# Kernel optimization log

Hardware: AMD Instinct MI355X
Metric: run time of the kernel (lower is better)

## Reference

```python
import jax, jax.numpy as jnp
import numpy as np

DT = 0.1
B, L, IN_SZ, MEM = 64, 2048, 128, 256


def setup_inputs() -> dict:
    key = jax.random.key(0)
    ks = jax.random.split(key, 13)
    u = jax.random.normal(ks[0], (B, L, IN_SZ), dtype=jnp.float32)
    s_in = 1.0 / np.sqrt(IN_SZ)
    s_h = 1.0 / np.sqrt(MEM)
    def w_in(k):
        return jax.random.normal(k, (MEM, IN_SZ), dtype=jnp.float32) * s_in
    def w_h(k):
        return jax.random.normal(k, (MEM, MEM), dtype=jnp.float32) * s_h
    return {
        "u": u,
        "Wia": w_in(ks[1]), "Wha": w_h(ks[2]),
        "Wib": w_in(ks[3]), "Whb": w_h(ks[4]),
        "Wic": w_in(ks[5]), "Whc": w_h(ks[6]),
        "Wid": w_in(ks[7]), "Whd": w_h(ks[8]),
        "Wie": w_in(ks[9]), "Whe": w_h(ks[10]),
        "Wio": w_in(ks[11]),
    }


def _run(u, Wia, Wha, Wib, Whb, Wic, Whc, Wid, Whd, Wie, Whe, Wio):
    # Precompute all 6 input projections once: [L, B, MEM] each (time-major for scan)
    Win = jnp.stack([Wia, Wib, Wic, Wid, Wie, Wio], axis=0)  # [6, MEM, IN]
    xproj = jnp.einsum("blk,gmk->lgbm", u, Win)  # [L, 6, B, MEM]

    hf0 = jnp.zeros((u.shape[0], Wha.shape[0]), dtype=u.dtype)
    hs0 = jnp.zeros_like(hf0)

    def step(carry, xs):
        hf, hs = carry
        xa, xb, xc, xd, xe, xo = xs[0], xs[1], xs[2], xs[3], xs[4], xs[5]
        a = 1.0 + jnp.tanh(xa + hf @ Wha.T)
        b = 1.5 * (1.0 + jnp.tanh(xb + hf @ Whb.T))
        c = 3.0 * DT + (1.0 - 3.0 * DT) * jax.nn.sigmoid(xc + hf @ Whc.T)
        d = 0.3 * DT * jax.nn.sigmoid(xd + hf @ Whd.T)
        e = 1.0 + jax.nn.sigmoid(xe + hf @ Whe.T)
        hfn = (1.0 - c) * hf + c * jnp.tanh(xo + (a + b * hf * hf - hs) * hf)
        hsn = hs * (1.0 - d) + d * (e * hf) ** 4
        return (hfn, hsn), hfn

    _, hseq = jax.lax.scan(step, (hf0, hs0), xproj)  # [L, B, MEM]
    hseq = jnp.transpose(hseq, (1, 0, 2))  # [B, L, MEM]
    return hseq


def reference(u, Wia, Wha, Wib, Whb, Wic, Whc, Wid, Whd, Wie, Whe, Wio):
    hseq = _run(u, Wia, Wha, Wib, Whb, Wic, Whc, Wid, Whd, Wie, Whe, Wio)
    return hseq, hseq[:, -1:, :]
```

## Files before the change

kernel.cpp:

```cpp
#include <hip/hip_runtime.h>
#include <hip/hip_fp16.h>

#define L_SEQ 2048
#define N_B   64
#define IN_K  128
#define MEM_N 256

typedef float    f32x4 __attribute__((ext_vector_type(4)));
typedef _Float16 f16x8 __attribute__((ext_vector_type(8)));
typedef unsigned u32x4 __attribute__((ext_vector_type(4)));

__device__ __forceinline__ float rcp_f(float x) { return __builtin_amdgcn_rcpf(x); }
__device__ __forceinline__ float tanh_f(float x) {
    return 1.0f - 2.0f * rcp_f(__expf(2.0f * x) + 1.0f);
}
__device__ __forceinline__ float sig_f(float x) {
    return rcp_f(1.0f + __expf(-x));
}

__device__ __forceinline__ void split8(const float* v, f16x8& hi, f16x8& lo) {
#pragma unroll
    for (int i = 0; i < 8; ++i) {
        _Float16 h = (_Float16)v[i];
        hi[i] = h;
        lo[i] = (_Float16)(v[i] - (float)h);
    }
}

__global__ void __launch_bounds__(256, 1)
befrc_scan(const float* __restrict__ u,
           const float* __restrict__ Wia, const float* __restrict__ Wha,
           const float* __restrict__ Wib, const float* __restrict__ Whb,
           const float* __restrict__ Wic, const float* __restrict__ Whc,
           const float* __restrict__ Wid, const float* __restrict__ Whd,
           const float* __restrict__ Wie, const float* __restrict__ Whe,
           const float* __restrict__ Wio,
           float* __restrict__ out,
           unsigned long long* __restrict__ pubq)
{
    const int wg  = blockIdx.x;
    const int g   = wg & 3;
    const int s   = wg >> 2;
    const int tid = threadIdx.x;
    const int w   = tid >> 6;
    const int l   = tid & 63;
    const int lq  = l >> 4;
    const int lr  = l & 15;

    __shared__ __align__(16) float red[2][6][4][16][20];

    const float* Wi[6] = {Wia, Wib, Wic, Wid, Wie, Wio};
    const float* Wh[5] = {Wha, Whb, Whc, Whd, Whe};

    const int mrow = s * 16 + lr;
    f16x8 whf_hi[5][2], whf_lo[5][2];
#pragma unroll
    for (int gg = 0; gg < 5; ++gg) {
#pragma unroll
        for (int cc = 0; cc < 2; ++cc) {
            const int k0 = (2 * w + cc) * 32 + lq * 4;
            const float* p = Wh[gg] + mrow * MEM_N + k0;
            float4 f0 = *(const float4*)p;
            float4 f1 = *(const float4*)(p + 16);
            float v[8] = {f0.x, f0.y, f0.z, f0.w, f1.x, f1.y, f1.z, f1.w};
            split8(v, whf_hi[gg][cc], whf_lo[gg][cc]);
        }
    }
    f16x8 wif_hi[6], wif_lo[6];
#pragma unroll
    for (int gg = 0; gg < 6; ++gg) {
        const int k0 = w * 32 + lq * 4;
        const float* p = Wi[gg] + mrow * IN_K + k0;
        float4 f0 = *(const float4*)p;
        float4 f1 = *(const float4*)(p + 16);
        float v[8] = {f0.x, f0.y, f0.z, f0.w, f1.x, f1.y, f1.z, f1.w};
        split8(v, wif_hi[gg], wif_lo[gg]);
    }

    const int eb    = tid >> 4;
    const int em    = tid & 15;
    const int bglob = g * 16 + eb;
    const int mglob = s * 16 + em;
    float hf_loc = 0.0f, hs_loc = 0.0f;

    const int  bfrag  = g * 16 + lr;
    const long u_base = (long)bfrag * L_SEQ * IN_K + w * 32 + lq * 4;
    const int  k0a    = (2 * w + 0) * 32 + lq * 4;
    const int  k0b    = (2 * w + 1) * 32 + lq * 4;

    u32x4 ua, ub2;
    {
        const float* up = u + u_base;
        asm volatile(
            "global_load_dwordx4 %0, %2, off\n\t"
            "global_load_dwordx4 %1, %3, off"
            : "=v"(ua), "=v"(ub2)
            : "v"(up), "v"(up + 16)
            : "memory");
    }

    float* const out_row = out + (long)bglob * L_SEQ * MEM_N + mglob;

#pragma clang loop unroll(disable)
    for (int t = 0; t < L_SEQ; ++t) {
        u32x4 r0, r1, r2, r3, r4, r5, r6, r7;
        {
            const unsigned tgt = (unsigned)t;
            const unsigned long long* pb =
                pubq + (size_t)(t & 1) * N_B * MEM_N + (size_t)bfrag * MEM_N;
            const unsigned long long* p0 = pb + k0a;
            const unsigned long long* p1 = pb + k0a + 16;
            const unsigned long long* p2 = pb + k0b;
            const unsigned long long* p3 = pb + k0b + 16;
            int spins = 0;
            for (;;) {
                asm volatile(
                    "global_load_dwordx4 %0, %8, off sc0 sc1\n\t"
                    "global_load_dwordx4 %1, %8, off offset:16 sc0 sc1\n\t"
                    "global_load_dwordx4 %2, %9, off sc0 sc1\n\t"
                    "global_load_dwordx4 %3, %9, off offset:16 sc0 sc1\n\t"
                    "global_load_dwordx4 %4, %10, off sc0 sc1\n\t"
                    "global_load_dwordx4 %5, %10, off offset:16 sc0 sc1\n\t"
                    "global_load_dwordx4 %6, %11, off sc0 sc1\n\t"
                    "global_load_dwordx4 %7, %11, off offset:16 sc0 sc1\n\t"
                    "s_waitcnt vmcnt(0)"
                    : "=v"(r0), "=v"(r1), "=v"(r2), "=v"(r3),
                      "=v"(r4), "=v"(r5), "=v"(r6), "=v"(r7)
                    : "v"(p0), "v"(p1), "v"(p2), "v"(p3)
                    : "memory");
                int ok = (r0[1] == tgt) & (r0[3] == tgt) & (r1[1] == tgt) & (r1[3] == tgt)
                       & (r2[1] == tgt) & (r2[3] == tgt) & (r3[1] == tgt) & (r3[3] == tgt)
                       & (r4[1] == tgt) & (r4[3] == tgt) & (r5[1] == tgt) & (r5[3] == tgt)
                       & (r6[1] == tgt) & (r6[3] == tgt) & (r7[1] == tgt) & (r7[3] == tgt);
                if (__all(ok) || ++spins > (1 << 17)) break;
            }
        }
        __builtin_amdgcn_sched_barrier(0);

        f32x4 acc[6];
#pragma unroll
        for (int gg = 0; gg < 6; ++gg) acc[gg] = (f32x4){0.f, 0.f, 0.f, 0.f};
        {
            float4 f0 = __builtin_bit_cast(float4, ua);
            float4 f1 = __builtin_bit_cast(float4, ub2);
            float v[8] = {f0.x, f0.y, f0.z, f0.w, f1.x, f1.y, f1.z, f1.w};
            f16x8 uh, ul;
            split8(v, uh, ul);
#pragma unroll
            for (int gg = 0; gg < 6; ++gg) {
                acc[gg] = __builtin_amdgcn_mfma_f32_16x16x32_f16(wif_hi[gg], uh, acc[gg], 0, 0, 0);
                acc[gg] = __builtin_amdgcn_mfma_f32_16x16x32_f16(wif_hi[gg], ul, acc[gg], 0, 0, 0);
                acc[gg] = __builtin_amdgcn_mfma_f32_16x16x32_f16(wif_lo[gg], uh, acc[gg], 0, 0, 0);
            }
        }

        {
            const float* up = u + u_base + (long)((t + 1 < L_SEQ) ? t + 1 : t) * IN_K;
            asm volatile(
                "global_load_dwordx4 %0, %2, off\n\t"
                "global_load_dwordx4 %1, %3, off"
                : "=v"(ua), "=v"(ub2)
                : "v"(up), "v"(up + 16)
                : "memory");
        }

        unsigned pay[16] = {r0[0], r0[2], r1[0], r1[2], r2[0], r2[2], r3[0], r3[2],
                            r4[0], r4[2], r5[0], r5[2], r6[0], r6[2], r7[0], r7[2]};
#pragma unroll
        for (int cc = 0; cc < 2; ++cc) {
            f16x8 hb_hi, hb_lo;
#pragma unroll
            for (int j = 0; j < 8; ++j) {
                const unsigned p = pay[cc * 8 + j];
                hb_hi[j] = __builtin_bit_cast(_Float16, (unsigned short)(p & 0xffff));
                hb_lo[j] = __builtin_bit_cast(_Float16, (unsigned short)(p >> 16));
            }
#pragma unroll
            for (int gg = 0; gg < 5; ++gg) {
                acc[gg] = __builtin_amdgcn_mfma_f32_16x16x32_f16(whf_hi[gg][cc], hb_hi, acc[gg], 0, 0, 0);
                acc[gg] = __builtin_amdgcn_mfma_f32_16x16x32_f16(whf_hi[gg][cc], hb_lo, acc[gg], 0, 0, 0);
                acc[gg] = __builtin_amdgcn_mfma_f32_16x16x32_f16(whf_lo[gg][cc], hb_hi, acc[gg], 0, 0, 0);
            }
        }

        const int pb2 = t & 1;
#pragma unroll
        for (int gg = 0; gg < 6; ++gg)
            *(f32x4*)&red[pb2][gg][w][lr][lq * 4] = acc[gg];
        asm volatile("s_waitcnt lgkmcnt(0)\n\ts_barrier" ::: "memory");
        __builtin_amdgcn_sched_barrier(0);

        float pre0, pre1, pre2, pre5;
        pre0 = red[pb2][0][0][eb][em] + red[pb2][0][1][eb][em]
             + red[pb2][0][2][eb][em] + red[pb2][0][3][eb][em];
        pre1 = red[pb2][1][0][eb][em] + red[pb2][1][1][eb][em]
             + red[pb2][1][2][eb][em] + red[pb2][1][3][eb][em];
        pre2 = red[pb2][2][0][eb][em] + red[pb2][2][1][eb][em]
             + red[pb2][2][2][eb][em] + red[pb2][2][3][eb][em];
        pre5 = red[pb2][5][0][eb][em] + red[pb2][5][1][eb][em]
             + red[pb2][5][2][eb][em] + red[pb2][5][3][eb][em];

        const float hf_old = hf_loc, hs_old = hs_loc;
        {
            const float av  = 1.0f + tanh_f(pre0);
            const float bv  = 1.5f * (1.0f + tanh_f(pre1));
            const float cv  = 0.3f  + 0.7f * sig_f(pre2);
            const float arg = pre5 + (av + bv * hf_old * hf_old - hs_old) * hf_old;
            hf_loc = (1.0f - cv) * hf_old + cv * tanh_f(arg);
        }
        {
            const _Float16 ph = (_Float16)hf_loc;
            const _Float16 pl = (_Float16)(hf_loc - (float)ph);
            const unsigned paw = (unsigned)__builtin_bit_cast(unsigned short, ph)
                               | ((unsigned)__builtin_bit_cast(unsigned short, pl) << 16);
            const unsigned long long val = ((unsigned long long)(unsigned)(t + 1) << 32) | paw;
            const size_t po = (size_t)((t + 1) & 1) * N_B * MEM_N
                            + (size_t)bglob * MEM_N + mglob;
            __hip_atomic_store(pubq + po, val, __ATOMIC_RELAXED, __HIP_MEMORY_SCOPE_AGENT);
        }

        {
            const float pre3 = red[pb2][3][0][eb][em] + red[pb2][3][1][eb][em]
                             + red[pb2][3][2][eb][em] + red[pb2][3][3][eb][em];
            const float pre4 = red[pb2][4][0][eb][em] + red[pb2][4][1][eb][em]
                             + red[pb2][4][2][eb][em] + red[pb2][4][3][eb][em];
            const float dv  = 0.03f * sig_f(pre3);
            const float ev  = 1.0f + sig_f(pre4);
            const float eh  = ev * hf_old;
            const float eh2 = eh * eh;
            hs_loc = hs_old * (1.0f - dv) + dv * (eh2 * eh2);
        }
        out_row[(long)t * MEM_N] = hf_loc;
    }

    out[(long)N_B * L_SEQ * MEM_N + (long)bglob * MEM_N + mglob] = hf_loc;
}

extern "C" void kernel_launch(void* const* d_in, const int* in_sizes, int n_in,
                              void* d_out, int out_size, void* d_ws, size_t ws_size,
                              hipStream_t stream) {
    (void)in_sizes; (void)n_in; (void)out_size; (void)ws_size;
    const float* u   = (const float*)d_in[0];
    const float* Wia = (const float*)d_in[1];
    const float* Wha = (const float*)d_in[2];
    const float* Wib = (const float*)d_in[3];
    const float* Whb = (const float*)d_in[4];
    const float* Wic = (const float*)d_in[5];
    const float* Whc = (const float*)d_in[6];
    const float* Wid = (const float*)d_in[7];
    const float* Whd = (const float*)d_in[8];
    const float* Wie = (const float*)d_in[9];
    const float* Whe = (const float*)d_in[10];
    const float* Wio = (const float*)d_in[11];

    float* out = (float*)d_out;
    unsigned long long* pubq = (unsigned long long*)d_ws;

    hipMemsetAsync(d_ws, 0, (size_t)2 * N_B * MEM_N * sizeof(unsigned long long), stream);

    befrc_scan<<<dim3(64), dim3(256), 0, stream>>>(
        u, Wia, Wha, Wib, Whb, Wic, Whc, Wid, Whd, Wie, Whe, Wio,
        out, pubq);
}
```

Measured before the change: 5.616 ms.

## Place workgroups on one XCC and use L2-coherent polling when co-located

The kernel now launches 512 workgroups and keeps only every eighth one, which tends to place the working groups on the same XCC. At startup the groups run a probe handshake that reads the XCC id and checks cross-group store visibility. If all peers in a batch group share one XCC, the per-step exchange switches from system-coherent (sc0 sc1) loads and atomic stores to sc0-only loads and plain stores, which avoids the slower cross-die coherence path. The output store of each step is also deferred into the next iteration so it sits off the critical path. The risks are the fragile placement assumption and the extra startup handshake; the kernel falls back to the old path if the check fails.

```diff
diff --git a/kernel.cpp b/kernel.cpp
--- a/kernel.cpp
+++ b/kernel.cpp
@@ -27,7 +27,7 @@
     }
 }
 
-__global__ void __launch_bounds__(256, 1)
+__global__ void __launch_bounds__(256, 2)
 befrc_scan(const float* __restrict__ u,
            const float* __restrict__ Wia, const float* __restrict__ Wha,
            const float* __restrict__ Wib, const float* __restrict__ Whb,
@@ -36,11 +36,14 @@
            const float* __restrict__ Wie, const float* __restrict__ Whe,
            const float* __restrict__ Wio,
            float* __restrict__ out,
-           unsigned long long* __restrict__ pubq)
+           unsigned long long* __restrict__ pubq,
+           unsigned* __restrict__ ctrl,
+           unsigned* __restrict__ probe)
 {
-    const int wg  = blockIdx.x;
-    const int g   = wg & 3;
-    const int s   = wg >> 2;
+    if (blockIdx.x & 7) return;
+    const int rwg = blockIdx.x >> 3;
+    const int g   = rwg & 3;
+    const int s   = rwg >> 2;
     const int tid = threadIdx.x;
     const int w   = tid >> 6;
     const int l   = tid & 63;
@@ -48,6 +51,49 @@
     const int lr  = l & 15;
 
     __shared__ __align__(16) float red[2][6][4][16][20];
+    __shared__ int s_fast;
+
+    unsigned xcc;
+    asm volatile("s_getreg_b32 %0, hwreg(HW_REG_XCC_ID)" : "=s"(xcc));
+    int ok = 1;
+    {
+        unsigned* myslot = probe + (unsigned)rwg * 16;
+        const unsigned* peer = probe + (unsigned)(g + 4 * (l & 15)) * 16;
+        for (int r = 1; r <= 4; ++r) {
+            if (tid == 0)
+                asm volatile("global_store_dword %0, %1, off"
+                             :: "v"(myslot), "v"(r) : "memory");
+            if (w == 0) {
+                int good = 0;
+                for (int it = 0; it < 2048; ++it) {
+                    unsigned v;
+                    asm volatile("global_load_dword %0, %1, off sc0\n\t"
+                                 "s_waitcnt vmcnt(0)"
+                                 : "=v"(v) : "v"(peer) : "memory");
+                    if (__all((int)(l >= 16 || v >= (unsigned)r))) { good = 1; break; }
+                }
+                ok &= good;
+            }
+        }
+    }
+    if (tid == 0)
+        __hip_atomic_store(&ctrl[rwg],
+                           0x10000u | ((unsigned)(ok & 1) << 8) | (xcc & 0xffu),
+                           __ATOMIC_RELEASE, __HIP_MEMORY_SCOPE_AGENT);
+    if (w == 0) {
+        unsigned v;
+        for (;;) {
+            v = __hip_atomic_load(&ctrl[g + 4 * (l & 15)],
+                                  __ATOMIC_ACQUIRE, __HIP_MEMORY_SCOPE_AGENT);
+            if (__all((int)((v & 0x10000u) != 0))) break;
+            __builtin_amdgcn_s_sleep(2);
+        }
+        const unsigned ref = __builtin_amdgcn_readfirstlane(v);
+        const int f = (__all((int)(v == ref)) && ((ref >> 8) & 1)) ? 1 : 0;
+        if (tid == 0) s_fast = f;
+    }
+    __syncthreads();
+    const bool fast = (s_fast != 0);
 
     const float* Wi[6] = {Wia, Wib, Wic, Wid, Wie, Wio};
     const float* Wh[5] = {Wha, Whb, Whc, Whd, Whe};
@@ -81,7 +127,7 @@
     const int em    = tid & 15;
     const int bglob = g * 16 + eb;
     const int mglob = s * 16 + em;
-    float hf_loc = 0.0f, hs_loc = 0.0f;
+    float hf_loc = 0.0f, hs_loc = 0.0f, h_prev = 0.0f;
 
     const int  bfrag  = g * 16 + lr;
     const long u_base = (long)bfrag * L_SEQ * IN_K + w * 32 + lq * 4;
@@ -113,29 +159,55 @@
             const unsigned long long* p2 = pb + k0b;
             const unsigned long long* p3 = pb + k0b + 16;
             int spins = 0;
-            for (;;) {
-                asm volatile(
-                    "global_load_dwordx4 %0, %8, off sc0 sc1\n\t"
-                    "global_load_dwordx4 %1, %8, off offset:16 sc0 sc1\n\t"
-                    "global_load_dwordx4 %2, %9, off sc0 sc1\n\t"
-                    "global_load_dwordx4 %3, %9, off offset:16 sc0 sc1\n\t"
-                    "global_load_dwordx4 %4, %10, off sc0 sc1\n\t"
-                    "global_load_dwordx4 %5, %10, off offset:16 sc0 sc1\n\t"
-                    "global_load_dwordx4 %6, %11, off sc0 sc1\n\t"
-                    "global_load_dwordx4 %7, %11, off offset:16 sc0 sc1\n\t"
-                    "s_waitcnt vmcnt(0)"
-                    : "=v"(r0), "=v"(r1), "=v"(r2), "=v"(r3),
-                      "=v"(r4), "=v"(r5), "=v"(r6), "=v"(r7)
-                    : "v"(p0), "v"(p1), "v"(p2), "v"(p3)
-                    : "memory");
-                int ok = (r0[1] == tgt) & (r0[3] == tgt) & (r1[1] == tgt) & (r1[3] == tgt)
-                       & (r2[1] == tgt) & (r2[3] == tgt) & (r3[1] == tgt) & (r3[3] == tgt)
-                       & (r4[1] == tgt) & (r4[3] == tgt) & (r5[1] == tgt) & (r5[3] == tgt)
-                       & (r6[1] == tgt) & (r6[3] == tgt) & (r7[1] == tgt) & (r7[3] == tgt);
-                if (__all(ok) || ++spins > (1 << 17)) break;
+            if (fast) {
+                for (;;) {
+                    asm volatile(
+                        "global_load_dwordx4 %0, %8, off sc0\n\t"
+                        "global_load_dwordx4 %1, %8, off offset:16 sc0\n\t"
+                        "global_load_dwordx4 %2, %9, off sc0\n\t"
+                        "global_load_dwordx4 %3, %9, off offset:16 sc0\n\t"
+                        "global_load_dwordx4 %4, %10, off sc0\n\t"
+                        "global_load_dwordx4 %5, %10, off offset:16 sc0\n\t"
+                        "global_load_dwordx4 %6, %11, off sc0\n\t"
+                        "global_load_dwordx4 %7, %11, off offset:16 sc0\n\t"
+                        "s_waitcnt vmcnt(0)"
+                        : "=v"(r0), "=v"(r1), "=v"(r2), "=v"(r3),
+                          "=v"(r4), "=v"(r5), "=v"(r6), "=v"(r7)
+                        : "v"(p0), "v"(p1), "v"(p2), "v"(p3)
+                        : "memory");
+                    int ok2 = (r0[1] == tgt) & (r0[3] == tgt) & (r1[1] == tgt) & (r1[3] == tgt)
+                            & (r2[1] == tgt) & (r2[3] == tgt) & (r3[1] == tgt) & (r3[3] == tgt)
+                            & (r4[1] == tgt) & (r4[3] == tgt) & (r5[1] == tgt) & (r5[3] == tgt)
+                            & (r6[1] == tgt) & (r6[3] == tgt) & (r7[1] == tgt) & (r7[3] == tgt);
+                    if (__all(ok2) || ++spins > (1 << 20)) break;
+                }
+            } else {
+                for (;;) {
+                    asm volatile(
+                        "global_load_dwordx4 %0, %8, off sc0 sc1\n\t"
+                        "global_load_dwordx4 %1, %8, off offset:16 sc0 sc1\n\t"
+                        "global_load_dwordx4 %2, %9, off sc0 sc1\n\t"
+                        "global_load_dwordx4 %3, %9, off offset:16 sc0 sc1\n\t"
+                        "global_load_dwordx4 %4, %10, off sc0 sc1\n\t"
+                        "global_load_dwordx4 %5, %10, off offset:16 sc0 sc1\n\t"
+                        "global_load_dwordx4 %6, %11, off sc0 sc1\n\t"
+                        "global_load_dwordx4 %7, %11, off offset:16 sc0 sc1\n\t"
+                        "s_waitcnt vmcnt(0)"
+                        : "=v"(r0), "=v"(r1), "=v"(r2), "=v"(r3),
+                          "=v"(r4), "=v"(r5), "=v"(r6), "=v"(r7)
+                        : "v"(p0), "v"(p1), "v"(p2), "v"(p3)
+                        : "memory");
+                    int ok2 = (r0[1] == tgt) & (r0[3] == tgt) & (r1[1] == tgt) & (r1[3] == tgt)
+                            & (r2[1] == tgt) & (r2[3] == tgt) & (r3[1] == tgt) & (r3[3] == tgt)
+                            & (r4[1] == tgt) & (r4[3] == tgt) & (r5[1] == tgt) & (r5[3] == tgt)
+                            & (r6[1] == tgt) & (r6[3] == tgt) & (r7[1] == tgt) & (r7[3] == tgt);
+                    if (__all(ok2) || ++spins > (1 << 17)) break;
+                }
             }
         }
         __builtin_amdgcn_sched_barrier(0);
+
+        if (t) out_row[(long)(t - 1) * MEM_N] = h_prev;
 
         f32x4 acc[6];
 #pragma unroll
@@ -214,9 +286,14 @@
             const unsigned paw = (unsigned)__builtin_bit_cast(unsigned short, ph)
                                | ((unsigned)__builtin_bit_cast(unsigned short, pl) << 16);
             const unsigned long long val = ((unsigned long long)(unsigned)(t + 1) << 32) | paw;
-            const size_t po = (size_t)((t + 1) & 1) * N_B * MEM_N
-                            + (size_t)bglob * MEM_N + mglob;
-            __hip_atomic_store(pubq + po, val, __ATOMIC_RELAXED, __HIP_MEMORY_SCOPE_AGENT);
+            unsigned long long* pp = pubq + (size_t)((t + 1) & 1) * N_B * MEM_N
+                                   + (size_t)bglob * MEM_N + mglob;
+            if (fast) {
+                asm volatile("global_store_dwordx2 %0, %1, off"
+                             :: "v"(pp), "v"(val) : "memory");
+            } else {
+                __hip_atomic_store(pp, val, __ATOMIC_RELAXED, __HIP_MEMORY_SCOPE_AGENT);
+            }
         }
 
         {
@@ -230,9 +307,10 @@
             const float eh2 = eh * eh;
             hs_loc = hs_old * (1.0f - dv) + dv * (eh2 * eh2);
         }
-        out_row[(long)t * MEM_N] = hf_loc;
-    }
-
+        h_prev = hf_loc;
+    }
+
+    out_row[(long)(L_SEQ - 1) * MEM_N] = hf_loc;
     out[(long)N_B * L_SEQ * MEM_N + (long)bglob * MEM_N + mglob] = hf_loc;
 }
 
@@ -255,10 +333,12 @@
 
     float* out = (float*)d_out;
     unsigned long long* pubq = (unsigned long long*)d_ws;
-
-    hipMemsetAsync(d_ws, 0, (size_t)2 * N_B * MEM_N * sizeof(unsigned long long), stream);
-
-    befrc_scan<<<dim3(64), dim3(256), 0, stream>>>(
+    unsigned* ctrl  = (unsigned*)((char*)d_ws + 262144);
+    unsigned* probe = (unsigned*)((char*)d_ws + 262400);
+
+    hipMemsetAsync(d_ws, 0, 262144 + 256 + 4096, stream);
+
+    befrc_scan<<<dim3(512), dim3(256), 0, stream>>>(
         u, Wia, Wha, Wib, Whb, Wic, Whc, Wid, Whd, Wie, Whe, Wio,
-        out, pubq);
-}
+        out, pubq, ctrl, probe);
+}
```

Measured after the change: 10.89 ms. 1.94x slower.

## Interleave four batch chunks per workgroup and prefetch published state into LDS

Applied to the files above, without the earlier changes.

The grid shrinks from 64 to 16 workgroups. Each workgroup now handles all four 16-row batch chunks in turn within a time step, so while one chunk computes, the other chunks' hidden-state publications have time to arrive. The published state layout is reorganised per chunk, and the next chunk's state is prefetched asynchronously into LDS with global_load_lds. Global spin-polling is used only when the prefetched data is stale. Output stores are deferred by one step. The cost is four times more serial work per workgroup and fewer CUs in use, in exchange for hiding cross-workgroup synchronisation latency.

```diff
diff --git a/kernel.cpp b/kernel.cpp
--- a/kernel.cpp
+++ b/kernel.cpp
@@ -9,6 +9,10 @@
 typedef float    f32x4 __attribute__((ext_vector_type(4)));
 typedef _Float16 f16x8 __attribute__((ext_vector_type(8)));
 typedef unsigned u32x4 __attribute__((ext_vector_type(4)));
+typedef unsigned u32x2 __attribute__((ext_vector_type(2)));
+
+typedef const __attribute__((address_space(1))) void gas_t;
+typedef __attribute__((address_space(3))) void las_t;
 
 __device__ __forceinline__ float rcp_f(float x) { return __builtin_amdgcn_rcpf(x); }
 __device__ __forceinline__ float tanh_f(float x) {
@@ -38,15 +42,14 @@
            float* __restrict__ out,
            unsigned long long* __restrict__ pubq)
 {
-    const int wg  = blockIdx.x;
-    const int g   = wg & 3;
-    const int s   = wg >> 2;
+    const int s   = blockIdx.x;
     const int tid = threadIdx.x;
     const int w   = tid >> 6;
     const int l   = tid & 63;
     const int lq  = l >> 4;
     const int lr  = l & 15;
 
+    __shared__ __align__(16) unsigned long long pref[2][4][1024];
     __shared__ __align__(16) float red[2][6][4][16][20];
 
     const float* Wi[6] = {Wia, Wib, Wic, Wid, Wie, Wio};
@@ -59,9 +62,9 @@
 #pragma unroll
         for (int cc = 0; cc < 2; ++cc) {
             const int k0 = (2 * w + cc) * 32 + lq * 4;
-            const float* p = Wh[gg] + mrow * MEM_N + k0;
-            float4 f0 = *(const float4*)p;
-            float4 f1 = *(const float4*)(p + 16);
+            const float* ptr = Wh[gg] + mrow * MEM_N + k0;
+            float4 f0 = *(const float4*)ptr;
+            float4 f1 = *(const float4*)(ptr + 16);
             float v[8] = {f0.x, f0.y, f0.z, f0.w, f1.x, f1.y, f1.z, f1.w};
             split8(v, whf_hi[gg][cc], whf_lo[gg][cc]);
         }
@@ -70,170 +73,238 @@
 #pragma unroll
     for (int gg = 0; gg < 6; ++gg) {
         const int k0 = w * 32 + lq * 4;
-        const float* p = Wi[gg] + mrow * IN_K + k0;
-        float4 f0 = *(const float4*)p;
-        float4 f1 = *(const float4*)(p + 16);
+        const float* ptr = Wi[gg] + mrow * IN_K + k0;
+        float4 f0 = *(const float4*)ptr;
+        float4 f1 = *(const float4*)(ptr + 16);
         float v[8] = {f0.x, f0.y, f0.z, f0.w, f1.x, f1.y, f1.z, f1.w};
         split8(v, wif_hi[gg], wif_lo[gg]);
     }
 
     const int eb    = tid >> 4;
     const int em    = tid & 15;
-    const int bglob = g * 16 + eb;
     const int mglob = s * 16 + em;
-    float hf_loc = 0.0f, hs_loc = 0.0f;
-
-    const int  bfrag  = g * 16 + lr;
-    const long u_base = (long)bfrag * L_SEQ * IN_K + w * 32 + lq * 4;
-    const int  k0a    = (2 * w + 0) * 32 + lq * 4;
-    const int  k0b    = (2 * w + 1) * 32 + lq * 4;
-
-    u32x4 ua, ub2;
+
+    float hfv[4] = {0.f, 0.f, 0.f, 0.f};
+    float hsv[4] = {0.f, 0.f, 0.f, 0.f};
+    float hpv[4] = {0.f, 0.f, 0.f, 0.f};
+    long  ub4[4];
+    float* orow[4];
+#pragma unroll
+    for (int c = 0; c < 4; ++c) {
+        ub4[c]  = (long)(c * 16 + lr) * L_SEQ * IN_K + w * 32 + lq * 4;
+        orow[c] = out + (long)(c * 16 + eb) * L_SEQ * MEM_N + mglob;
+    }
+    u32x4 upA[2], upB[2];
+
     {
-        const float* up = u + u_base;
+        const float* up = u + ub4[0];
         asm volatile(
             "global_load_dwordx4 %0, %2, off\n\t"
             "global_load_dwordx4 %1, %3, off"
-            : "=v"(ua), "=v"(ub2)
+            : "=v"(upA[0]), "=v"(upB[0])
             : "v"(up), "v"(up + 16)
             : "memory");
-    }
-
-    float* const out_row = out + (long)bglob * L_SEQ * MEM_N + mglob;
+        const char* gp = (const char*)(pubq + (size_t)w * 1024) + ((unsigned)l << 4);
+#pragma unroll
+        for (int ch = 0; ch < 8; ++ch)
+            __builtin_amdgcn_global_load_lds(
+                (gas_t*)(gp + ch * 1024),
+                (las_t*)((char*)&pref[0][w][0] + ch * 1024), 16, 0, 17);
+    }
 
 #pragma clang loop unroll(disable)
     for (int t = 0; t < L_SEQ; ++t) {
-        u32x4 r0, r1, r2, r3, r4, r5, r6, r7;
-        {
+#pragma unroll
+        for (int c = 0; c < 4; ++c) {
+            const int par = c & 1;
+            const int nc  = (c + 1) & 3;
+            const int ntt = (c == 3) ? (t + 1) : t;
             const unsigned tgt = (unsigned)t;
-            const unsigned long long* pb =
-                pubq + (size_t)(t & 1) * N_B * MEM_N + (size_t)bfrag * MEM_N;
-            const unsigned long long* p0 = pb + k0a;
-            const unsigned long long* p1 = pb + k0a + 16;
-            const unsigned long long* p2 = pb + k0b;
-            const unsigned long long* p3 = pb + k0b + 16;
-            int spins = 0;
-            for (;;) {
+
+            asm volatile("s_waitcnt vmcnt(0)" ::: "memory");
+            __builtin_amdgcn_sched_barrier(0);
+
+            if (t) orow[c][(long)(t - 1) * MEM_N] = hpv[c];
+
+            unsigned long long qv[16];
+            {
+                const unsigned long long* lp = &pref[par][w][(unsigned)(lq * 64 + lr)];
+#pragma unroll
+                for (int blk = 0; blk < 4; ++blk)
+#pragma unroll
+                    for (int i = 0; i < 4; ++i)
+                        qv[blk * 4 + i] = lp[blk * 256 + i * 16];
+            }
+            int okt = 1;
+#pragma unroll
+            for (int i = 0; i < 16; ++i)
+                okt &= ((unsigned)(qv[i] >> 32) == tgt);
+
+            if (!__all(okt)) {
+                const unsigned long long* gb =
+                    pubq + (((size_t)(t & 1)) * 4 + c) * 4096
+                         + (size_t)w * 1024 + (unsigned)(lq * 64 + lr);
+                const unsigned long long* gb0 = gb;
+                const unsigned long long* gb1 = gb + 256;
+                const unsigned long long* gb2 = gb + 512;
+                const unsigned long long* gb3 = gb + 768;
+                int spins = 0;
+                for (;;) {
+                    u32x2 m0, m1, m2, m3, m4, m5, m6, m7,
+                          m8, m9, m10, m11, m12, m13, m14, m15;
+                    asm volatile(
+                        "global_load_dwordx2 %0, %16, off sc0 sc1\n\t"
+                        "global_load_dwordx2 %1, %16, off offset:128 sc0 sc1\n\t"
+                        "global_load_dwordx2 %2, %16, off offset:256 sc0 sc1\n\t"
+                        "global_load_dwordx2 %3, %16, off offset:384 sc0 sc1\n\t"
+                        "global_load_dwordx2 %4, %17, off sc0 sc1\n\t"
+                        "global_load_dwordx2 %5, %17, off offset:128 sc0 sc1\n\t"
+                        "global_load_dwordx2 %6, %17, off offset:256 sc0 sc1\n\t"
+                        "global_load_dwordx2 %7, %17, off offset:384 sc0 sc1\n\t"
+                        "global_load_dwordx2 %8, %18, off sc0 sc1\n\t"
+                        "global_load_dwordx2 %9, %18, off offset:128 sc0 sc1\n\t"
+                        "global_load_dwordx2 %10, %18, off offset:256 sc0 sc1\n\t"
+                        "global_load_dwordx2 %11, %18, off offset:384 sc0 sc1\n\t"
+                        "global_load_dwordx2 %12, %19, off sc0 sc1\n\t"
+                        "global_load_dwordx2 %13, %19, off offset:128 sc0 sc1\n\t"
+                        "global_load_dwordx2 %14, %19, off offset:256 sc0 sc1\n\t"
+                        "global_load_dwordx2 %15, %19, off offset:384 sc0 sc1\n\t"
+                        "s_waitcnt vmcnt(0)"
+                        : "=v"(m0), "=v"(m1), "=v"(m2), "=v"(m3),
+                          "=v"(m4), "=v"(m5), "=v"(m6), "=v"(m7),
+                          "=v"(m8), "=v"(m9), "=v"(m10), "=v"(m11),
+                          "=v"(m12), "=v"(m13), "=v"(m14), "=v"(m15)
+                        : "v"(gb0), "v"(gb1), "v"(gb2), "v"(gb3)
+                        : "memory");
+                    int ok2 = (m0[1] == tgt) & (m1[1] == tgt) & (m2[1] == tgt) & (m3[1] == tgt)
+                            & (m4[1] == tgt) & (m5[1] == tgt) & (m6[1] == tgt) & (m7[1] == tgt)
+                            & (m8[1] == tgt) & (m9[1] == tgt) & (m10[1] == tgt) & (m11[1] == tgt)
+                            & (m12[1] == tgt) & (m13[1] == tgt) & (m14[1] == tgt) & (m15[1] == tgt);
+                    if (__all(ok2) || ++spins > (1 << 17)) {
+                        u32x2 mm[16] = {m0, m1, m2, m3, m4, m5, m6, m7,
+                                        m8, m9, m10, m11, m12, m13, m14, m15};
+#pragma unroll
+                        for (int i = 0; i < 16; ++i)
+                            qv[i] = ((unsigned long long)mm[i][1] << 32) | mm[i][0];
+                        break;
+                    }
+                }
+            }
+            __builtin_amdgcn_sched_barrier(0);
+
+            {
+                const char* gp = (const char*)(pubq
+                        + (((size_t)(ntt & 1)) * 4 + nc) * 4096
+                        + (size_t)w * 1024) + ((unsigned)l << 4);
+                char* ld = (char*)&pref[par ^ 1][w][0];
+#pragma unroll
+                for (int ch = 0; ch < 8; ++ch)
+                    __builtin_amdgcn_global_load_lds(
+                        (gas_t*)(gp + ch * 1024),
+                        (las_t*)(ld + ch * 1024), 16, 0, 17);
+            }
+            {
+                const float* up = u + ub4[nc]
+                                + (long)((ntt < L_SEQ) ? ntt : (L_SEQ - 1)) * IN_K;
                 asm volatile(
-                    "global_load_dwordx4 %0, %8, off sc0 sc1\n\t"
-                    "global_load_dwordx4 %1, %8, off offset:16 sc0 sc1\n\t"
-                    "global_load_dwordx4 %2, %9, off sc0 sc1\n\t"
-                    "global_load_dwordx4 %3, %9, off offset:16 sc0 sc1\n\t"
-                    "global_load_dwordx4 %4, %10, off sc0 sc1\n\t"
-                    "global_load_dwordx4 %5, %10, off offset:16 sc0 sc1\n\t"
-                    "global_load_dwordx4 %6, %11, off sc0 sc1\n\t"
-                    "global_load_dwordx4 %7, %11, off offset:16 sc0 sc1\n\t"
-                    "s_waitcnt vmcnt(0)"
-                    : "=v"(r0), "=v"(r1), "=v"(r2), "=v"(r3),
-                      "=v"(r4), "=v"(r5), "=v"(r6), "=v"(r7)
-                    : "v"(p0), "v"(p1), "v"(p2), "v"(p3)
+                    "global_load_dwordx4 %0, %2, off\n\t"
+                    "global_load_dwordx4 %1, %3, off"
+                    : "=v"(upA[par ^ 1]), "=v"(upB[par ^ 1])
+                    : "v"(up), "v"(up + 16)
                     : "memory");
-                int ok = (r0[1] == tgt) & (r0[3] == tgt) & (r1[1] == tgt) & (r1[3] == tgt)
-                       & (r2[1] == tgt) & (r2[3] == tgt) & (r3[1] == tgt) & (r3[3] == tgt)
-                       & (r4[1] == tgt) & (r4[3] == tgt) & (r5[1] == tgt) & (r5[3] == tgt)
-                       & (r6[1] == tgt) & (r6[3] == tgt) & (r7[1] == tgt) & (r7[3] == tgt);
-                if (__all(ok) || ++spins > (1 << 17)) break;
-            }
+            }
+
+            f32x4 acc[6];
+#pragma unroll
+            for (int gg = 0; gg < 6; ++gg) acc[gg] = (f32x4){0.f, 0.f, 0.f, 0.f};
+            {
+                float4 f0 = __builtin_bit_cast(float4, upA[par]);
+                float4 f1 = __builtin_bit_cast(float4, upB[par]);
+                float v[8] = {f0.x, f0.y, f0.z, f0.w, f1.x, f1.y, f1.z, f1.w};
+                f16x8 uh, ul;
+                split8(v, uh, ul);
+#pragma unroll
+                for (int gg = 0; gg < 6; ++gg) {
+                    acc[gg] = __builtin_amdgcn_mfma_f32_16x16x32_f16(wif_hi[gg], uh, acc[gg], 0, 0, 0);
+                    acc[gg] = __builtin_amdgcn_mfma_f32_16x16x32_f16(wif_hi[gg], ul, acc[gg], 0, 0, 0);
+                    acc[gg] = __builtin_amdgcn_mfma_f32_16x16x32_f16(wif_lo[gg], uh, acc[gg], 0, 0, 0);
+                }
+            }
+
+#pragma unroll
+            for (int cc = 0; cc < 2; ++cc) {
+                f16x8 hb_hi, hb_lo;
+#pragma unroll
+                for (int j = 0; j < 8; ++j) {
+                    const unsigned pv = (unsigned)qv[(2 * cc + (j >> 2)) * 4 + (j & 3)];
+                    hb_hi[j] = __builtin_bit_cast(_Float16, (unsigned short)(pv & 0xffff));
+                    hb_lo[j] = __builtin_bit_cast(_Float16, (unsigned short)(pv >> 16));
+                }
+#pragma unroll
+                for (int gg = 0; gg < 5; ++gg) {
+                    acc[gg] = __builtin_amdgcn_mfma_f32_16x16x32_f16(whf_hi[gg][cc], hb_hi, acc[gg], 0, 0, 0);
+                    acc[gg] = __builtin_amdgcn_mfma_f32_16x16x32_f16(whf_hi[gg][cc], hb_lo, acc[gg], 0, 0, 0);
+                    acc[gg] = __builtin_amdgcn_mfma_f32_16x16x32_f16(whf_lo[gg][cc], hb_hi, acc[gg], 0, 0, 0);
+                }
+            }
+
+#pragma unroll
+            for (int gg = 0; gg < 6; ++gg)
+                *(f32x4*)&red[par][gg][w][lr][lq * 4] = acc[gg];
+            asm volatile("s_waitcnt lgkmcnt(0)\n\ts_barrier" ::: "memory");
+            __builtin_amdgcn_sched_barrier(0);
+
+            const float pre0 = red[par][0][0][eb][em] + red[par][0][1][eb][em]
+                             + red[par][0][2][eb][em] + red[par][0][3][eb][em];
+            const float pre1 = red[par][1][0][eb][em] + red[par][1][1][eb][em]
+                             + red[par][1][2][eb][em] + red[par][1][3][eb][em];
+            const float pre2 = red[par][2][0][eb][em] + red[par][2][1][eb][em]
+                             + red[par][2][2][eb][em] + red[par][2][3][eb][em];
+            const float pre5 = red[par][5][0][eb][em] + red[par][5][1][eb][em]
+                             + red[par][5][2][eb][em] + red[par][5][3][eb][em];
+
+            const float hf_old = hfv[c], hs_old = hsv[c];
+            float hfn;
+            {
+                const float av  = 1.0f + tanh_f(pre0);
+                const float bv  = 1.5f * (1.0f + tanh_f(pre1));
+                const float cv  = 0.3f + 0.7f * sig_f(pre2);
+                const float arg = pre5 + (av + bv * hf_old * hf_old - hs_old) * hf_old;
+                hfn = (1.0f - cv) * hf_old + cv * tanh_f(arg);
+            }
+            hfv[c] = hfn;
+            {
+                const _Float16 ph = (_Float16)hfn;
+                const _Float16 pl = (_Float16)(hfn - (float)ph);
+                const unsigned paw = (unsigned)__builtin_bit_cast(unsigned short, ph)
+                                   | ((unsigned)__builtin_bit_cast(unsigned short, pl) << 16);
+                const unsigned long long val =
+                    ((unsigned long long)(unsigned)(t + 1) << 32) | paw;
+                unsigned long long* pp = pubq
+                    + (((size_t)((t + 1) & 1)) * 4 + c) * 4096
+                    + (size_t)mglob * 16 + eb;
+                __hip_atomic_store(pp, val, __ATOMIC_RELAXED, __HIP_MEMORY_SCOPE_AGENT);
+            }
+            {
+                const float pre3 = red[par][3][0][eb][em] + red[par][3][1][eb][em]
+                                 + red[par][3][2][eb][em] + red[par][3][3][eb][em];
+                const float pre4 = red[par][4][0][eb][em] + red[par][4][1][eb][em]
+                                 + red[par][4][2][eb][em] + red[par][4][3][eb][em];
+                const float dv  = 0.03f * sig_f(pre3);
+                const float ev  = 1.0f + sig_f(pre4);
+                const float eh  = ev * hf_old;
+                const float eh2 = eh * eh;
+                hsv[c] = hs_old * (1.0f - dv) + dv * (eh2 * eh2);
+            }
+            hpv[c] = hfn;
         }
-        __builtin_amdgcn_sched_barrier(0);
-
-        f32x4 acc[6];
-#pragma unroll
-        for (int gg = 0; gg < 6; ++gg) acc[gg] = (f32x4){0.f, 0.f, 0.f, 0.f};
-        {
-            float4 f0 = __builtin_bit_cast(float4, ua);
-            float4 f1 = __builtin_bit_cast(float4, ub2);
-            float v[8] = {f0.x, f0.y, f0.z, f0.w, f1.x, f1.y, f1.z, f1.w};
-            f16x8 uh, ul;
-            split8(v, uh, ul);
-#pragma unroll
-            for (int gg = 0; gg < 6; ++gg) {
-                acc[gg] = __builtin_amdgcn_mfma_f32_16x16x32_f16(wif_hi[gg], uh, acc[gg], 0, 0, 0);
-                acc[gg] = __builtin_amdgcn_mfma_f32_16x16x32_f16(wif_hi[gg], ul, acc[gg], 0, 0, 0);
-                acc[gg] = __builtin_amdgcn_mfma_f32_16x16x32_f16(wif_lo[gg], uh, acc[gg], 0, 0, 0);
-            }
-        }
-
-        {
-            const float* up = u + u_base + (long)((t + 1 < L_SEQ) ? t + 1 : t) * IN_K;
-            asm volatile(
-                "global_load_dwordx4 %0, %2, off\n\t"
-                "global_load_dwordx4 %1, %3, off"
-                : "=v"(ua), "=v"(ub2)
-                : "v"(up), "v"(up + 16)
-                : "memory");
-        }
-
-        unsigned pay[16] = {r0[0], r0[2], r1[0], r1[2], r2[0], r2[2], r3[0], r3[2],
-                            r4[0], r4[2], r5[0], r5[2], r6[0], r6[2], r7[0], r7[2]};
-#pragma unroll
-        for (int cc = 0; cc < 2; ++cc) {
-            f16x8 hb_hi, hb_lo;
-#pragma unroll
-            for (int j = 0; j < 8; ++j) {
-                const unsigned p = pay[cc * 8 + j];
-                hb_hi[j] = __builtin_bit_cast(_Float16, (unsigned short)(p & 0xffff));
-                hb_lo[j] = __builtin_bit_cast(_Float16, (unsigned short)(p >> 16));
-            }
-#pragma unroll
-            for (int gg = 0; gg < 5; ++gg) {
-                acc[gg] = __builtin_amdgcn_mfma_f32_16x16x32_f16(whf_hi[gg][cc], hb_hi, acc[gg], 0, 0, 0);
-                acc[gg] = __builtin_amdgcn_mfma_f32_16x16x32_f16(whf_hi[gg][cc], hb_lo, acc[gg], 0, 0, 0);
-                acc[gg] = __builtin_amdgcn_mfma_f32_16x16x32_f16(whf_lo[gg][cc], hb_hi, acc[gg], 0, 0, 0);
-            }
-        }
-
-        const int pb2 = t & 1;
-#pragma unroll
-        for (int gg = 0; gg < 6; ++gg)
-            *(f32x4*)&red[pb2][gg][w][lr][lq * 4] = acc[gg];
-        asm volatile("s_waitcnt lgkmcnt(0)\n\ts_barrier" ::: "memory");
-        __builtin_amdgcn_sched_barrier(0);
-
-        float pre0, pre1, pre2, pre5;
-        pre0 = red[pb2][0][0][eb][em] + red[pb2][0][1][eb][em]
-             + red[pb2][0][2][eb][em] + red[pb2][0][3][eb][em];
-        pre1 = red[pb2][1][0][eb][em] + red[pb2][1][1][eb][em]
-             + red[pb2][1][2][eb][em] + red[pb2][1][3][eb][em];
-        pre2 = red[pb2][2][0][eb][em] + red[pb2][2][1][eb][em]
-             + red[pb2][2][2][eb][em] + red[pb2][2][3][eb][em];
-        pre5 = red[pb2][5][0][eb][em] + red[pb2][5][1][eb][em]
-             + red[pb2][5][2][eb][em] + red[pb2][5][3][eb][em];
-
-        const float hf_old = hf_loc, hs_old = hs_loc;
-        {
-            const float av  = 1.0f + tanh_f(pre0);
-            const float bv  = 1.5f * (1.0f + tanh_f(pre1));
-            const float cv  = 0.3f  + 0.7f * sig_f(pre2);
-            const float arg = pre5 + (av + bv * hf_old * hf_old - hs_old) * hf_old;
-            hf_loc = (1.0f - cv) * hf_old + cv * tanh_f(arg);
-        }
-        {
-            const _Float16 ph = (_Float16)hf_loc;
-            const _Float16 pl = (_Float16)(hf_loc - (float)ph);
-            const unsigned paw = (unsigned)__builtin_bit_cast(unsigned short, ph)
-                               | ((unsigned)__builtin_bit_cast(unsigned short, pl) << 16);
-            const unsigned long long val = ((unsigned long long)(unsigned)(t + 1) << 32) | paw;
-            const size_t po = (size_t)((t + 1) & 1) * N_B * MEM_N
-                            + (size_t)bglob * MEM_N + mglob;
-            __hip_atomic_store(pubq + po, val, __ATOMIC_RELAXED, __HIP_MEMORY_SCOPE_AGENT);
-        }
-
-        {
-            const float pre3 = red[pb2][3][0][eb][em] + red[pb2][3][1][eb][em]
-                             + red[pb2][3][2][eb][em] + red[pb2][3][3][eb][em];
-            const float pre4 = red[pb2][4][0][eb][em] + red[pb2][4][1][eb][em]
-                             + red[pb2][4][2][eb][em] + red[pb2][4][3][eb][em];
-            const float dv  = 0.03f * sig_f(pre3);
-            const float ev  = 1.0f + sig_f(pre4);
-            const float eh  = ev * hf_old;
-            const float eh2 = eh * eh;
-            hs_loc = hs_old * (1.0f - dv) + dv * (eh2 * eh2);
-        }
-        out_row[(long)t * MEM_N] = hf_loc;
-    }
-
-    out[(long)N_B * L_SEQ * MEM_N + (long)bglob * MEM_N + mglob] = hf_loc;
+    }
+
+#pragma unroll
+    for (int c = 0; c < 4; ++c) {
+        orow[c][(long)(L_SEQ - 1) * MEM_N] = hfv[c];
+        out[(long)N_B * L_SEQ * MEM_N + (long)(c * 16 + eb) * MEM_N + mglob] = hfv[c];
+    }
 }
 
 extern "C" void kernel_launch(void* const* d_in, const int* in_sizes, int n_in,
@@ -256,9 +327,9 @@
     float* out = (float*)d_out;
     unsigned long long* pubq = (unsigned long long*)d_ws;
 
-    hipMemsetAsync(d_ws, 0, (size_t)2 * N_B * MEM_N * sizeof(unsigned long long), stream);
-
-    befrc_scan<<<dim3(64), dim3(256), 0, stream>>>(
+    hipMemsetAsync(d_ws, 0, (size_t)2 * 4 * 256 * 16 * sizeof(unsigned long long), stream);
+
+    befrc_scan<<<dim3(16), dim3(256), 0, stream>>>(
         u, Wia, Wha, Wib, Whb, Wic, Whc, Wid, Whd, Wie, Whe, Wio,
         out, pubq);
 }
```

New measurement: 15.97 ms. 2.84x slower.

## Issue next-step flag loads early and defer output stores in recurrent loop

Applied to the files above, without the earlier changes.

The first poll of the next step's published hidden-state flags is now issued right after this step's own publish store, so its latency overlaps the hs update and the next step's input MFMAs instead of sitting on the critical path. A slow spin loop runs only when that early read is stale. The output store for step t is deferred to the next iteration so the store issue does not delay the loop tail. The LDS reduction buffer row padding also changes from 20 to 17 floats, with the vector stores turned into scalar stores, to change bank-conflict behaviour. The early read will often be stale, which can add an extra poll round trip.

```diff
diff --git a/kernel.cpp b/kernel.cpp
--- a/kernel.cpp
+++ b/kernel.cpp
@@ -47,7 +47,7 @@
     const int lq  = l >> 4;
     const int lr  = l & 15;
 
-    __shared__ __align__(16) float red[2][6][4][16][20];
+    __shared__ __align__(16) float red[2][6][4][16][17];
 
     const float* Wi[6] = {Wia, Wib, Wic, Wid, Wie, Wio};
     const float* Wh[5] = {Wha, Whb, Whc, Whd, Whe};
@@ -59,9 +59,9 @@
 #pragma unroll
         for (int cc = 0; cc < 2; ++cc) {
             const int k0 = (2 * w + cc) * 32 + lq * 4;
-            const float* p = Wh[gg] + mrow * MEM_N + k0;
-            float4 f0 = *(const float4*)p;
-            float4 f1 = *(const float4*)(p + 16);
+            const float* ptr = Wh[gg] + mrow * MEM_N + k0;
+            float4 f0 = *(const float4*)ptr;
+            float4 f1 = *(const float4*)(ptr + 16);
             float v[8] = {f0.x, f0.y, f0.z, f0.w, f1.x, f1.y, f1.z, f1.w};
             split8(v, whf_hi[gg][cc], whf_lo[gg][cc]);
         }
@@ -70,9 +70,9 @@
 #pragma unroll
     for (int gg = 0; gg < 6; ++gg) {
         const int k0 = w * 32 + lq * 4;
-        const float* p = Wi[gg] + mrow * IN_K + k0;
-        float4 f0 = *(const float4*)p;
-        float4 f1 = *(const float4*)(p + 16);
+        const float* ptr = Wi[gg] + mrow * IN_K + k0;
+        float4 f0 = *(const float4*)ptr;
+        float4 f1 = *(const float4*)(ptr + 16);
         float v[8] = {f0.x, f0.y, f0.z, f0.w, f1.x, f1.y, f1.z, f1.w};
         split8(v, wif_hi[gg], wif_lo[gg]);
     }
@@ -81,12 +81,14 @@
     const int em    = tid & 15;
     const int bglob = g * 16 + eb;
     const int mglob = s * 16 + em;
-    float hf_loc = 0.0f, hs_loc = 0.0f;
+    float hf_loc = 0.0f, hs_loc = 0.0f, h_prev = 0.0f;
 
     const int  bfrag  = g * 16 + lr;
     const long u_base = (long)bfrag * L_SEQ * IN_K + w * 32 + lq * 4;
     const int  k0a    = (2 * w + 0) * 32 + lq * 4;
     const int  k0b    = (2 * w + 1) * 32 + lq * 4;
+
+    u32x4 r0, r1, r2, r3, r4, r5, r6, r7;
 
     u32x4 ua, ub2;
     {
@@ -97,45 +99,67 @@
             : "=v"(ua), "=v"(ub2)
             : "v"(up), "v"(up + 16)
             : "memory");
+        const unsigned long long* pb = pubq + (size_t)bfrag * MEM_N;
+        asm volatile(
+            "global_load_dwordx4 %0, %8, off sc0 sc1\n\t"
+            "global_load_dwordx4 %1, %8, off offset:16 sc0 sc1\n\t"
+            "global_load_dwordx4 %2, %9, off sc0 sc1\n\t"
+            "global_load_dwordx4 %3, %9, off offset:16 sc0 sc1\n\t"
+            "global_load_dwordx4 %4, %10, off sc0 sc1\n\t"
+            "global_load_dwordx4 %5, %10, off offset:16 sc0 sc1\n\t"
+            "global_load_dwordx4 %6, %11, off sc0 sc1\n\t"
+            "global_load_dwordx4 %7, %11, off offset:16 sc0 sc1"
+            : "=v"(r0), "=v"(r1), "=v"(r2), "=v"(r3),
+              "=v"(r4), "=v"(r5), "=v"(r6), "=v"(r7)
+            : "v"(pb + k0a), "v"(pb + k0a + 16), "v"(pb + k0b), "v"(pb + k0b + 16)
+            : "memory");
     }
 
     float* const out_row = out + (long)bglob * L_SEQ * MEM_N + mglob;
 
 #pragma clang loop unroll(disable)
     for (int t = 0; t < L_SEQ; ++t) {
-        u32x4 r0, r1, r2, r3, r4, r5, r6, r7;
-        {
-            const unsigned tgt = (unsigned)t;
-            const unsigned long long* pb =
-                pubq + (size_t)(t & 1) * N_B * MEM_N + (size_t)bfrag * MEM_N;
-            const unsigned long long* p0 = pb + k0a;
-            const unsigned long long* p1 = pb + k0a + 16;
-            const unsigned long long* p2 = pb + k0b;
-            const unsigned long long* p3 = pb + k0b + 16;
-            int spins = 0;
-            for (;;) {
-                asm volatile(
-                    "global_load_dwordx4 %0, %8, off sc0 sc1\n\t"
-                    "global_load_dwordx4 %1, %8, off offset:16 sc0 sc1\n\t"
-                    "global_load_dwordx4 %2, %9, off sc0 sc1\n\t"
-                    "global_load_dwordx4 %3, %9, off offset:16 sc0 sc1\n\t"
-                    "global_load_dwordx4 %4, %10, off sc0 sc1\n\t"
-                    "global_load_dwordx4 %5, %10, off offset:16 sc0 sc1\n\t"
-                    "global_load_dwordx4 %6, %11, off sc0 sc1\n\t"
-                    "global_load_dwordx4 %7, %11, off offset:16 sc0 sc1\n\t"
-                    "s_waitcnt vmcnt(0)"
-                    : "=v"(r0), "=v"(r1), "=v"(r2), "=v"(r3),
-                      "=v"(r4), "=v"(r5), "=v"(r6), "=v"(r7)
-                    : "v"(p0), "v"(p1), "v"(p2), "v"(p3)
-                    : "memory");
-                int ok = (r0[1] == tgt) & (r0[3] == tgt) & (r1[1] == tgt) & (r1[3] == tgt)
-                       & (r2[1] == tgt) & (r2[3] == tgt) & (r3[1] == tgt) & (r3[3] == tgt)
-                       & (r4[1] == tgt) & (r4[3] == tgt) & (r5[1] == tgt) & (r5[3] == tgt)
-                       & (r6[1] == tgt) & (r6[3] == tgt) & (r7[1] == tgt) & (r7[3] == tgt);
-                if (__all(ok) || ++spins > (1 << 17)) break;
+        const unsigned tgt = (unsigned)t;
+        const unsigned long long* pb =
+            pubq + (size_t)(t & 1) * N_B * MEM_N + (size_t)bfrag * MEM_N;
+
+        asm volatile("s_waitcnt vmcnt(0)" ::: "memory");
+        __builtin_amdgcn_sched_barrier(0);
+
+        {
+            int ok2 = (r0[1] == tgt) & (r0[3] == tgt) & (r1[1] == tgt) & (r1[3] == tgt)
+                    & (r2[1] == tgt) & (r2[3] == tgt) & (r3[1] == tgt) & (r3[3] == tgt)
+                    & (r4[1] == tgt) & (r4[3] == tgt) & (r5[1] == tgt) & (r5[3] == tgt)
+                    & (r6[1] == tgt) & (r6[3] == tgt) & (r7[1] == tgt) & (r7[3] == tgt);
+            if (!__all(ok2)) {
+                int spins = 0;
+                for (;;) {
+                    asm volatile(
+                        "global_load_dwordx4 %0, %8, off sc0 sc1\n\t"
+                        "global_load_dwordx4 %1, %8, off offset:16 sc0 sc1\n\t"
+                        "global_load_dwordx4 %2, %9, off sc0 sc1\n\t"
+                        "global_load_dwordx4 %3, %9, off offset:16 sc0 sc1\n\t"
+                        "global_load_dwordx4 %4, %10, off sc0 sc1\n\t"
+                        "global_load_dwordx4 %5, %10, off offset:16 sc0 sc1\n\t"
+                        "global_load_dwordx4 %6, %11, off sc0 sc1\n\t"
+                        "global_load_dwordx4 %7, %11, off offset:16 sc0 sc1\n\t"
+                        "s_waitcnt vmcnt(0)"
+                        : "=v"(r0), "=v"(r1), "=v"(r2), "=v"(r3),
+                          "=v"(r4), "=v"(r5), "=v"(r6), "=v"(r7)
+                        : "v"(pb + k0a), "v"(pb + k0a + 16),
+                          "v"(pb + k0b), "v"(pb + k0b + 16)
+                        : "memory");
+                    int ok3 = (r0[1] == tgt) & (r0[3] == tgt) & (r1[1] == tgt) & (r1[3] == tgt)
+                            & (r2[1] == tgt) & (r2[3] == tgt) & (r3[1] == tgt) & (r3[3] == tgt)
+                            & (r4[1] == tgt) & (r4[3] == tgt) & (r5[1] == tgt) & (r5[3] == tgt)
+                            & (r6[1] == tgt) & (r6[3] == tgt) & (r7[1] == tgt) & (r7[3] == tgt);
+                    if (__all(ok3) || ++spins > (1 << 17)) break;
+                }
             }
         }
         __builtin_amdgcn_sched_barrier(0);
+
+        if (t) out_row[(long)(t - 1) * MEM_N] = h_prev;
 
         f32x4 acc[6];
 #pragma unroll
@@ -171,9 +195,9 @@
             f16x8 hb_hi, hb_lo;
 #pragma unroll
             for (int j = 0; j < 8; ++j) {
-                const unsigned p = pay[cc * 8 + j];
-                hb_hi[j] = __builtin_bit_cast(_Float16, (unsigned short)(p & 0xffff));
-                hb_lo[j] = __builtin_bit_cast(_Float16, (unsigned short)(p >> 16));
+                const unsigned pv = pay[cc * 8 + j];
+                hb_hi[j] = __builtin_bit_cast(_Float16, (unsigned short)(pv & 0xffff));
+                hb_lo[j] = __builtin_bit_cast(_Float16, (unsigned short)(pv >> 16));
             }
 #pragma unroll
             for (int gg = 0; gg < 5; ++gg) {
@@ -186,19 +210,20 @@
         const int pb2 = t & 1;
 #pragma unroll
         for (int gg = 0; gg < 6; ++gg)
-            *(f32x4*)&red[pb2][gg][w][lr][lq * 4] = acc[gg];
+#pragma unroll
+            for (int i = 0; i < 4; ++i)
+                red[pb2][gg][w][lr][lq * 4 + i] = acc[gg][i];
         asm volatile("s_waitcnt lgkmcnt(0)\n\ts_barrier" ::: "memory");
         __builtin_amdgcn_sched_barrier(0);
 
-        float pre0, pre1, pre2, pre5;
-        pre0 = red[pb2][0][0][eb][em] + red[pb2][0][1][eb][em]
-             + red[pb2][0][2][eb][em] + red[pb2][0][3][eb][em];
-        pre1 = red[pb2][1][0][eb][em] + red[pb2][1][1][eb][em]
-             + red[pb2][1][2][eb][em] + red[pb2][1][3][eb][em];
-        pre2 = red[pb2][2][0][eb][em] + red[pb2][2][1][eb][em]
-             + red[pb2][2][2][eb][em] + red[pb2][2][3][eb][em];
-        pre5 = red[pb2][5][0][eb][em] + red[pb2][5][1][eb][em]
-             + red[pb2][5][2][eb][em] + red[pb2][5][3][eb][em];
+        const float pre0 = red[pb2][0][0][eb][em] + red[pb2][0][1][eb][em]
+                         + red[pb2][0][2][eb][em] + red[pb2][0][3][eb][em];
+        const float pre1 = red[pb2][1][0][eb][em] + red[pb2][1][1][eb][em]
+                         + red[pb2][1][2][eb][em] + red[pb2][1][3][eb][em];
+        const float pre2 = red[pb2][2][0][eb][em] + red[pb2][2][1][eb][em]
+                         + red[pb2][2][2][eb][em] + red[pb2][2][3][eb][em];
+        const float pre5 = red[pb2][5][0][eb][em] + red[pb2][5][1][eb][em]
+                         + red[pb2][5][2][eb][em] + red[pb2][5][3][eb][em];
 
         const float hf_old = hf_loc, hs_old = hs_loc;
         {
@@ -214,9 +239,26 @@
             const unsigned paw = (unsigned)__builtin_bit_cast(unsigned short, ph)
                                | ((unsigned)__builtin_bit_cast(unsigned short, pl) << 16);
             const unsigned long long val = ((unsigned long long)(unsigned)(t + 1) << 32) | paw;
-            const size_t po = (size_t)((t + 1) & 1) * N_B * MEM_N
-                            + (size_t)bglob * MEM_N + mglob;
-            __hip_atomic_store(pubq + po, val, __ATOMIC_RELAXED, __HIP_MEMORY_SCOPE_AGENT);
+            unsigned long long* pp = pubq + (size_t)((t + 1) & 1) * N_B * MEM_N
+                                   + (size_t)bglob * MEM_N + mglob;
+            __hip_atomic_store(pp, val, __ATOMIC_RELAXED, __HIP_MEMORY_SCOPE_AGENT);
+        }
+        if (t + 1 < L_SEQ) {
+            const unsigned long long* pn =
+                pubq + (size_t)((t + 1) & 1) * N_B * MEM_N + (size_t)bfrag * MEM_N;
+            asm volatile(
+                "global_load_dwordx4 %0, %8, off sc0 sc1\n\t"
+                "global_load_dwordx4 %1, %8, off offset:16 sc0 sc1\n\t"
+                "global_load_dwordx4 %2, %9, off sc0 sc1\n\t"
+                "global_load_dwordx4 %3, %9, off offset:16 sc0 sc1\n\t"
+                "global_load_dwordx4 %4, %10, off sc0 sc1\n\t"
+                "global_load_dwordx4 %5, %10, off offset:16 sc0 sc1\n\t"
+                "global_load_dwordx4 %6, %11, off sc0 sc1\n\t"
+                "global_load_dwordx4 %7, %11, off offset:16 sc0 sc1"
+                : "=v"(r0), "=v"(r1), "=v"(r2), "=v"(r3),
+                  "=v"(r4), "=v"(r5), "=v"(r6), "=v"(r7)
+                : "v"(pn + k0a), "v"(pn + k0a + 16), "v"(pn + k0b), "v"(pn + k0b + 16)
+                : "memory");
         }
 
         {
@@ -230,9 +272,10 @@
             const float eh2 = eh * eh;
             hs_loc = hs_old * (1.0f - dv) + dv * (eh2 * eh2);
         }
-        out_row[(long)t * MEM_N] = hf_loc;
-    }
-
+        h_prev = hf_loc;
+    }
+
+    out_row[(long)(L_SEQ - 1) * MEM_N] = hf_loc;
     out[(long)N_B * L_SEQ * MEM_N + (long)bglob * MEM_N + mglob] = hf_loc;
 }
 
```

Result: slower. 6.878 ms (+22.5%).
